# Kernel tuning notes

Hardware: AMD Instinct MI355X
Metric: run time of the kernel (lower is better)

Reference implementation:

```python
import jax, jax.numpy as jnp
import numpy as np

EPS = 1e-5
P = 3  # p_size
BW = 1.0  # bandwidth


def _instance_norm(x):
    # calc_mean_std: per (B,C) mean/std over spatial dims, unbiased var (torch default)
    b, c, h, w = x.shape
    flat = x.reshape(b, c, h * w)
    mean = flat.mean(-1)[:, :, None, None]
    std = jnp.sqrt(flat.var(-1, ddof=1) + EPS)[:, :, None, None]
    return (x - mean) / std


def _conv1x1(x, w, bias):
    # x: (B,C,H,W), w: (O,C), bias: (O,)
    return jnp.einsum('oc,bchw->bohw', w, x) + bias[None, :, None, None]


def _patches_scaled(x, scale):
    # ReflectionPad2d(1) + Unfold(3) -> (B, HW, C*9), torch layout (c slow, k fast),
    # with ContextAtten scale applied over the 9 kernel positions.
    b, c, h, w = x.shape
    pad = jnp.pad(x, ((0, 0), (0, 0), (1, 1), (1, 1)), mode='reflect')
    # (B,C,H,W,9)
    p9 = jnp.stack([pad[:, :, di:di + h, dj:dj + w]
                    for di in range(P) for dj in range(P)], axis=-1)
    p9 = p9 * scale  # broadcast over last (kernel) axis
    # -> (B,H,W,C,9) -> (B, HW, C*9)
    return p9.transpose(0, 2, 3, 1, 4).reshape(b, h * w, c * P * P)


def setup_inputs() -> dict:
    key = jax.random.key(0)
    ks = jax.random.split(key, 12)
    B, C, H, W = 2, 512, 64, 64
    IC = 256
    f32 = jnp.float32
    inp = {
        'content': jax.random.normal(ks[0], (B, C, H, W), f32),
        'style': jax.random.normal(ks[1], (B, C, H, W), f32),
        'fusion_style': jax.random.normal(ks[2], (B, C, H, W), f32),
        'theta_w': jax.random.normal(ks[3], (IC, C), f32) * np.sqrt(2.0 / C),
        'theta_b': jnp.zeros((IC,), f32),
        'phi_w': jax.random.normal(ks[4], (IC, C), f32) * np.sqrt(2.0 / C),
        'phi_b': jnp.zeros((IC,), f32),
        'g_w': jax.random.normal(ks[5], (IC, C), f32) * np.sqrt(2.0 / C),
        'g_b': jnp.zeros((IC,), f32),
        'W_w': jax.random.normal(ks[6], (C, IC), f32) * np.sqrt(2.0 / IC),
        'W_b': jnp.zeros((C,), f32),
        'scale': jnp.ones((P * P,), f32),
    }
    return inp


def reference(content, style, fusion_style, theta_w, theta_b, phi_w, phi_b,
              g_w, g_b, W_w, W_b, scale):
    B, C, H, W = content.shape
    IC = theta_w.shape[0]
    HW = H * W

    # g on fusion_style -> (B, HW, IC)
    g_s = _conv1x1(fusion_style, g_w, g_b).reshape(B, IC, HW).transpose(0, 2, 1)

    # instance-normalize content/style (normal=True path)
    xn = _instance_norm(content)
    sn = _instance_norm(style)

    theta_x = _conv1x1(xn, theta_w, theta_b)
    phi_s = _conv1x1(sn, phi_w, phi_b)

    theta_p = _patches_scaled(theta_x, scale)  # (B, HW, IC*9)
    phi_p = _patches_scaled(phi_s, scale)      # (B, HW, IC*9)

    f = jnp.einsum('blk,bmk->blm', theta_p, phi_p) * BW  # (B, HW, HW)
    f_div_C = jax.nn.softmax(f, axis=-1)

    y = jnp.einsum('blm,bmo->blo', f_div_C, g_s)  # (B, HW, IC)
    y = y.transpose(0, 2, 1).reshape(B, IC, H, W)
    W_y = _conv1x1(y, W_w, W_b)  # (B, C, H, W)
    # isTraining=True path: conf_map = 0
    return W_y
```

## Files before the change

kernel.cpp:

```cpp
#include <hip/hip_runtime.h>
#include <stdint.h>

typedef __attribute__((ext_vector_type(8))) __bf16 bf16x8;
typedef __attribute__((ext_vector_type(4))) float f32x4;
typedef __attribute__((ext_vector_type(4))) unsigned int uint4v;
typedef __attribute__((ext_vector_type(4))) unsigned short ushort4v;
typedef __attribute__((ext_vector_type(8))) unsigned short ushort8v;

__device__ __forceinline__ float bf2f(unsigned short u){
  unsigned int x = ((unsigned int)u) << 16;
  return __builtin_bit_cast(float, x);
}
__device__ __forceinline__ unsigned short f2bf(float f){
  unsigned int x = __builtin_bit_cast(unsigned int, f);
  x += 0x7FFFu + ((x >> 16) & 1u);
  return (unsigned short)(x >> 16);
}

#define OUT_PART 4
#define OUT_PARTH 5

typedef const __attribute__((address_space(1))) unsigned int* gas1_t;
typedef __attribute__((address_space(3))) unsigned int* las3_t;
__device__ __forceinline__ void gload16(const void* g, void* l){
  __builtin_amdgcn_global_load_lds((gas1_t)g, (las3_t)l, 16, 0, 0);
}

template<int OM>
__global__ __launch_bounds__(256)
void gemm_bt(const unsigned short* __restrict__ A, int lda,
             const unsigned short* __restrict__ Bt, int ldb,
             int kchunk, void* __restrict__ Out, int ldo,
             size_t zStride, size_t aBatch, size_t bBatch,
             int sMask, int sShift)
{
  __shared__ uint4v AsmBuf[1024];
  __shared__ uint4v BsmBuf[1024];
  char* Asm = (char*)AsmBuf;
  char* Bsm = (char*)BsmBuf;

  const int tid  = threadIdx.x;
  const int lane = tid & 63;
  const int wave = tid >> 6;
  const int wy = wave >> 1, wx = wave & 1;
  const int lm = lane & 15, quad = lane >> 4;
  const int tileM = blockIdx.y * 128;
  const int tileN = blockIdx.x * 128;
  const int z = blockIdx.z;
  const int slice = z & sMask;
  const int batch = z >> sShift;

  A  += (size_t)slice*kchunk + (size_t)batch*aBatch;
  Bt += (size_t)slice*kchunk + (size_t)batch*bBatch;

  const int sr0 = tid >> 2, sc0 = tid & 3;
  const int sr1 = sr0 + 64;
  const size_t gA0 = (size_t)(tileM + sr0)*lda + ((sc0 ^ ((sr0 >> 1) & 3)) << 3);
  const size_t gA1 = (size_t)(tileM + sr1)*lda + ((sc0 ^ ((sr1 >> 1) & 3)) << 3);
  const size_t gB0 = (size_t)(tileN + sr0)*ldb + ((sc0 ^ ((sr0 >> 1) & 3)) << 3);
  const size_t gB1 = (size_t)(tileN + sr1)*ldb + ((sc0 ^ ((sr1 >> 1) & 3)) << 3);
  const int lOff0 = sr0*64 + sc0*16;
  const int lOff1 = sr1*64 + sc0*16;

  int aOff[4], bOff[4];
#pragma unroll
  for (int t = 0; t < 4; ++t){
    int ra = wy*64 + t*16 + lm;
    aOff[t] = ra*64 + ((quad ^ ((ra >> 1) & 3)) << 4);
    int rb = wx*64 + t*16 + lm;
    bOff[t] = rb*64 + ((quad ^ ((rb >> 1) & 3)) << 4);
  }

  f32x4 acc[4][4] = {};

  const int ksteps = kchunk >> 5;
  uint4v a0v = *(const uint4v*)(A + gA0);
  uint4v a1v = *(const uint4v*)(A + gA1);
  uint4v b0v = *(const uint4v*)(Bt + gB0);
  uint4v b1v = *(const uint4v*)(Bt + gB1);

  for (int kt = 0; kt < ksteps; ++kt){
    char* As = Asm + (kt & 1)*8192;
    char* Bs = Bsm + (kt & 1)*8192;
    *(uint4v*)(As + lOff0) = a0v;
    *(uint4v*)(As + lOff1) = a1v;
    *(uint4v*)(Bs + lOff0) = b0v;
    *(uint4v*)(Bs + lOff1) = b1v;
    __syncthreads();
    if (kt + 1 < ksteps){
      const unsigned short* Ak = A + (kt + 1)*32;
      const unsigned short* Bk = Bt + (kt + 1)*32;
      a0v = *(const uint4v*)(Ak + gA0);
      a1v = *(const uint4v*)(Ak + gA1);
      b0v = *(const uint4v*)(Bk + gB0);
      b1v = *(const uint4v*)(Bk + gB1);
    }
    bf16x8 af[4], bfr[4];
#pragma unroll
    for (int t = 0; t < 4; ++t){
      af[t]  = __builtin_bit_cast(bf16x8, *(const uint4v*)(As + aOff[t]));
      bfr[t] = __builtin_bit_cast(bf16x8, *(const uint4v*)(Bs + bOff[t]));
    }
#pragma unroll
    for (int tm = 0; tm < 4; ++tm)
#pragma unroll
      for (int tn = 0; tn < 4; ++tn)
        acc[tm][tn] = __builtin_amdgcn_mfma_f32_16x16x32_bf16(af[tm], bfr[tn], acc[tm][tn], 0, 0, 0);
  }

#pragma unroll
  for (int tm = 0; tm < 4; ++tm){
    const int rowb = tileM + wy*64 + tm*16 + quad*4;
#pragma unroll
    for (int tn = 0; tn < 4; ++tn){
      const int col = tileN + wx*64 + tn*16 + lm;
#pragma unroll
      for (int r = 0; r < 4; ++r){
        const float v = acc[tm][tn][r];
        const size_t idx = (size_t)z*zStride + (size_t)(rowb + r)*ldo + col;
        if (OM == OUT_PART) ((float*)Out)[idx] = v;
        else                ((unsigned short*)Out)[idx] = f2bf(v);
      }
    }
  }
}

template<int OM>
__global__ __launch_bounds__(256)
void gemm_wide(const unsigned short* __restrict__ A, int lda,
               const unsigned short* __restrict__ Bt, int ldb,
               int kchunk, void* __restrict__ Out, int ldo,
               size_t zStride, size_t aBatch, size_t bBatch,
               int sMask, int sShift)
{
  __shared__ char lds[49152];

  const int tid  = threadIdx.x;
  const int lane = tid & 63;
  const int wave = tid >> 6;
  const int wy = wave >> 1, wx = wave & 1;
  const int lm = lane & 15, quad = lane >> 4;
  const int tileM = blockIdx.y * 128;
  const int tileN = blockIdx.x * 256;
  const int z = blockIdx.z;
  const int slice = z & sMask;
  const int batch = z >> sShift;

  A  += (size_t)slice*kchunk + (size_t)batch*aBatch;
  Bt += (size_t)slice*kchunk + (size_t)batch*bBatch;

  const int srow  = tid >> 2;
  const int selem = (((tid & 3) ^ ((tid >> 3) & 3)) << 3);
  const int dst   = tid << 4;
  size_t gA[2], gB[4];
#pragma unroll
  for (int i = 0; i < 2; ++i)
    gA[i] = (size_t)(tileM + srow + 64*i)*lda + selem;
#pragma unroll
  for (int i = 0; i < 4; ++i)
    gB[i] = (size_t)(tileN + srow + 64*i)*ldb + selem;

  int aOff[4], bOff[8];
#pragma unroll
  for (int t = 0; t < 4; ++t){
    const int ra = wy*64 + t*16 + lm;
    aOff[t] = ra*64 + ((quad ^ ((ra >> 1) & 3)) << 4);
  }
#pragma unroll
  for (int t = 0; t < 8; ++t){
    const int rb = wx*128 + t*16 + lm;
    bOff[t] = rb*64 + ((quad ^ ((rb >> 1) & 3)) << 4);
  }

  f32x4 acc[4][8] = {};
  const int nk = kchunk >> 5;

#pragma unroll
  for (int i = 0; i < 2; ++i) gload16(A  + gA[i], lds + i*4096 + dst);
#pragma unroll
  for (int i = 0; i < 4; ++i) gload16(Bt + gB[i], lds + 8192 + i*4096 + dst);

  for (int kt = 0; kt < nk; ++kt){
    const char* As = lds + (kt & 1)*24576;
    const char* Bs = As + 8192;
    if (kt + 1 < nk){
      char* nbuf = lds + ((kt + 1) & 1)*24576;
      const unsigned short* Ak = A  + (size_t)(kt + 1)*32;
      const unsigned short* Bk = Bt + (size_t)(kt + 1)*32;
#pragma unroll
      for (int i = 0; i < 2; ++i) gload16(Ak + gA[i], nbuf + i*4096 + dst);
#pragma unroll
      for (int i = 0; i < 4; ++i) gload16(Bk + gB[i], nbuf + 8192 + i*4096 + dst);
      asm volatile("s_waitcnt vmcnt(6)" ::: "memory");
    } else {
      asm volatile("s_waitcnt vmcnt(0)" ::: "memory");
    }
    __builtin_amdgcn_s_barrier();
    asm volatile("" ::: "memory");

    bf16x8 af[4], bfr[8];
#pragma unroll
    for (int t = 0; t < 8; ++t)
      bfr[t] = __builtin_bit_cast(bf16x8, *(const uint4v*)(Bs + bOff[t]));
#pragma unroll
    for (int t = 0; t < 4; ++t)
      af[t] = __builtin_bit_cast(bf16x8, *(const uint4v*)(As + aOff[t]));
#pragma unroll
    for (int tm = 0; tm < 4; ++tm)
#pragma unroll
      for (int tn = 0; tn < 8; ++tn)
        acc[tm][tn] = __builtin_amdgcn_mfma_f32_16x16x32_bf16(af[tm], bfr[tn], acc[tm][tn], 0, 0, 0);

    asm volatile("" ::: "memory");
    __builtin_amdgcn_s_barrier();
  }

#pragma unroll
  for (int tm = 0; tm < 4; ++tm){
    const int rowb = tileM + wy*64 + tm*16 + quad*4;
#pragma unroll
    for (int tn = 0; tn < 8; ++tn){
      const int col = tileN + wx*128 + tn*16 + lm;
#pragma unroll
      for (int r = 0; r < 4; ++r){
        const float v = acc[tm][tn][r];
        const size_t idx = (size_t)z*zStride + (size_t)(rowb + r)*ldo + col;
        if (OM == OUT_PART) ((float*)Out)[idx] = v;
        else                ((unsigned short*)Out)[idx] = f2bf(v);
      }
    }
  }
}

__global__ __launch_bounds__(512, 2)
void gemm_big256(const unsigned short* __restrict__ A, int lda,
                 const unsigned short* __restrict__ Bt, int ldb,
                 int K, float* __restrict__ Out, int ldo,
                 size_t aBatch, size_t bBatch, size_t oBatch)
{
  __shared__ char lds[131072];

  const int tid  = threadIdx.x;
  const int lane = tid & 63;
  const int wv   = tid >> 6;
  const int wy = wv >> 2, wx = wv & 3;
  const int lm = lane & 15, quad = lane >> 4;

  const int lid = (int)(blockIdx.x + (blockIdx.y << 4) + (blockIdx.z << 8));
  const int swz = ((lid & 7) << 6) + (lid >> 3);
  const int tileM = ((swz >> 4) & 15) * 256;
  const int tileN = (swz & 15) * 256;
  const int z = swz >> 8;

  A   += (size_t)z*aBatch;
  Bt  += (size_t)z*bBatch;
  Out += (size_t)z*oBatch;

  const int srow  = tid >> 3;
  const int selem = (((tid & 7) ^ ((tid >> 3) & 7)) << 3);
  const int dst   = tid << 4;
  size_t gA[4], gB[4];
#pragma unroll
  for (int i = 0; i < 4; ++i){
    gA[i] = (size_t)(tileM + srow + 64*i)*lda + selem;
    gB[i] = (size_t)(tileN + srow + 64*i)*ldb + selem;
  }

  int xq[2];
#pragma unroll
  for (int kk = 0; kk < 2; ++kk)
    xq[kk] = ((((kk << 2) + quad) ^ (lm & 7)) << 4);
  const int aBase = (wy*128 + lm) << 7;
  const int bBase = (wx*64  + lm) << 7;

  f32x4 acc[8][4] = {};
  const int nk = K >> 6;

#pragma unroll
  for (int i = 0; i < 4; ++i) gload16(A  + gA[i], lds + i*8192 + dst);
#pragma unroll
  for (int i = 0; i < 4; ++i) gload16(Bt + gB[i], lds + 32768 + i*8192 + dst);

  for (int kt = 0; kt < nk; ++kt){
    const char* As = lds + (kt & 1)*65536;
    const char* Bs = As + 32768;
    if (kt + 1 < nk){
      char* nbuf = lds + ((kt + 1) & 1)*65536;
      const unsigned short* Ak = A  + (size_t)(kt + 1)*64;
      const unsigned short* Bk = Bt + (size_t)(kt + 1)*64;
#pragma unroll
      for (int i = 0; i < 4; ++i) gload16(Ak + gA[i], nbuf + i*8192 + dst);
#pragma unroll
      for (int i = 0; i < 4; ++i) gload16(Bk + gB[i], nbuf + 32768 + i*8192 + dst);
      asm volatile("s_waitcnt vmcnt(8)" ::: "memory");
    } else {
      asm volatile("s_waitcnt vmcnt(0)" ::: "memory");
    }
    __builtin_amdgcn_s_barrier();
    asm volatile("" ::: "memory");

#pragma unroll
    for (int kk = 0; kk < 2; ++kk){
      bf16x8 af[8], bfr[4];
#pragma unroll
      for (int n = 0; n < 4; ++n)
        bfr[n] = __builtin_bit_cast(bf16x8, *(const uint4v*)(Bs + bBase + n*2048 + xq[kk]));
#pragma unroll
      for (int m = 0; m < 8; ++m)
        af[m] = __builtin_bit_cast(bf16x8, *(const uint4v*)(As + aBase + m*2048 + xq[kk]));
#pragma unroll
      for (int m = 0; m < 8; ++m)
#pragma unroll
        for (int n = 0; n < 4; ++n)
          acc[m][n] = __builtin_amdgcn_mfma_f32_16x16x32_bf16(af[m], bfr[n], acc[m][n], 0, 0, 0);
    }

    asm volatile("" ::: "memory");
    __builtin_amdgcn_s_barrier();
  }

#pragma unroll
  for (int tm = 0; tm < 8; ++tm){
    const int rowb = tileM + wy*128 + tm*16 + quad*4;
#pragma unroll
    for (int tn = 0; tn < 4; ++tn){
      const int col = tileN + wx*64 + tn*16 + lm;
#pragma unroll
      for (int r = 0; r < 4; ++r)
        Out[(size_t)(rowb + r)*ldo + col] = acc[tm][tn][r];
    }
  }
}

__global__ __launch_bounds__(256)
void reduce_tp(const float* __restrict__ part,
               const float* __restrict__ tb, const float* __restrict__ pb,
               unsigned short* __restrict__ th, unsigned short* __restrict__ ph)
{
  const size_t i4 = ((size_t)blockIdx.x*256 + threadIdx.x) * 4;
  const int which = (int)(i4 >> 21);
  const size_t j = i4 & 0x1FFFFFu;
  const int col = (int)(j & 255u);
  f32x4 v = {0.f, 0.f, 0.f, 0.f};
#pragma unroll
  for (int s = 0; s < 4; ++s){
    f32x4 p = *(const f32x4*)&part[(size_t)((which << 2) + s)*2097152 + j];
#pragma unroll
    for (int e = 0; e < 4; ++e) v[e] += p[e];
  }
  f32x4 bv = *(const f32x4*)&(which ? pb : tb)[col];
  ushort4v hi, lo;
#pragma unroll
  for (int e = 0; e < 4; ++e){
    const float t = v[e] + bv[e];
    hi[e] = f2bf(t);
    lo[e] = f2bf(t - bf2f(hi[e]));
  }
  const size_t o = (j >> 8)*768 + col;
  unsigned short* O = which ? ph : th;
  const int dup = which ? 512 : 256;
  const int loo = which ? 256 : 512;
  *(ushort4v*)&O[o] = hi;
  *(ushort4v*)&O[o + dup] = hi;
  *(ushort4v*)&O[o + loo] = lo;
}

__global__ __launch_bounds__(256)
void reduce_g(const unsigned short* __restrict__ part,
              const float* __restrict__ gb, unsigned short* __restrict__ gs)
{
  const size_t i8 = ((size_t)blockIdx.x*256 + threadIdx.x) * 8;
  float v[8] = {};
#pragma unroll
  for (int s = 0; s < 4; ++s){
    uint4v u = *(const uint4v*)&part[(size_t)s*2097152 + i8];
#pragma unroll
    for (int e = 0; e < 8; ++e)
      v[e] += bf2f((unsigned short)((e & 1) ? (u[e >> 1] >> 16) : (u[e >> 1] & 0xffffu)));
  }
  const float gbv = gb[i8 >> 13];
  ushort8v o;
#pragma unroll
  for (int e = 0; e < 8; ++e) o[e] = f2bf(v[e] + gbv);
  *(ushort8v*)&gs[i8] = o;
}

__global__ __launch_bounds__(256)
void reduce_y(const unsigned short* __restrict__ part,
              unsigned short* __restrict__ yb)
{
  const size_t i8 = ((size_t)blockIdx.x*256 + threadIdx.x) * 8;
  const int b = (int)(i8 >> 20);
  const size_t j = i8 & 0xFFFFFu;
  float v[8] = {};
#pragma unroll
  for (int s = 0; s < 8; ++s){
    uint4v u = *(const uint4v*)&part[(size_t)((b << 3) + s)*1048576 + j];
#pragma unroll
    for (int e = 0; e < 8; ++e)
      v[e] += bf2f((unsigned short)((e & 1) ? (u[e >> 1] >> 16) : (u[e >> 1] & 0xffffu)));
  }
  ushort8v o;
#pragma unroll
  for (int e = 0; e < 8; ++e) o[e] = f2bf(v[e]);
  *(ushort8v*)&yb[i8] = o;
}

__global__ __launch_bounds__(256)
void reduce_w(const float* __restrict__ part, const float* __restrict__ wb,
              void* __restrict__ Out, const unsigned int* __restrict__ flagPtr)
{
  const size_t i4 = ((size_t)blockIdx.x*256 + threadIdx.x) * 4;
  const int b = (int)(i4 >> 21);
  const size_t j = i4 & 0x1FFFFFu;
  f32x4 p0 = *(const f32x4*)&part[(size_t)(b << 1)*2097152 + j];
  f32x4 p1 = *(const f32x4*)&part[(size_t)((b << 1) | 1)*2097152 + j];
  const float w = wb[(i4 >> 12) & 511u];
  f32x4 v;
#pragma unroll
  for (int e = 0; e < 4; ++e) v[e] = p0[e] + p1[e] + w;
  if (flagPtr[0]){
    *(f32x4*)&((float*)Out)[i4] = v;
  } else {
    ushort4v o;
#pragma unroll
    for (int e = 0; e < 4; ++e) o[e] = f2bf(v[e]);
    *(ushort4v*)&((unsigned short*)Out)[i4] = o;
  }
}

__global__ __launch_bounds__(256)
void detect_prep(const void* __restrict__ content,
                 const void* tb, const void* pb, const void* gb, const void* wb,
                 const void* sc,
                 unsigned int* __restrict__ flag, float* __restrict__ scale_c,
                 float* tb_c, float* pb_c, float* gb_c, float* wb_c)
{
  __shared__ int cnt;
  __shared__ unsigned int flg;
  const int tid = threadIdx.x;
  if (tid == 0) cnt = 0;
  __syncthreads();
  unsigned int w = ((const unsigned int*)content)[tid];
  int e = (w >> 23) & 0xFF;
  if (e >= 0x70 && e <= 0x8F) atomicAdd(&cnt, 1);
  __syncthreads();
  if (tid == 0){ flg = (cnt >= 128) ? 1u : 0u; flag[0] = flg; }
  __syncthreads();
  const unsigned int f = flg;
  auto rd = [&](const void* p, int i)->float{
    return f ? ((const float*)p)[i] : bf2f(((const unsigned short*)p)[i]);
  };
  if (tid < 9) scale_c[tid] = rd(sc, tid);
  tb_c[tid] = rd(tb, tid);
  pb_c[tid] = rd(pb, tid);
  gb_c[tid] = rd(gb, tid);
  wb_c[tid] = rd(wb, tid);
  wb_c[tid + 256] = rd(wb, tid + 256);
}

__global__ __launch_bounds__(256)
void conv_weights(const void* tw, const void* pw, const void* gw, const void* www,
                  const unsigned int* __restrict__ flagPtr,
                  unsigned short* __restrict__ wdup,
                  unsigned short* __restrict__ gwc,
                  unsigned short* __restrict__ wwc)
{
  const unsigned int fl = flagPtr[0];
  const int sec = blockIdx.y;
  const int idx = blockIdx.x*256 + threadIdx.x;
  auto rd = [&](const void* p, int i)->float{
    return fl ? ((const float*)p)[i] : bf2f(((const unsigned short*)p)[i]);
  };
  if (sec < 2){
    const void* w = sec ? pw : tw;
    const int o = idx >> 9, c = idx & 511;
    float v = rd(w, o*512 + c);
    unsigned short hi = f2bf(v);
    unsigned short lo = f2bf(v - bf2f(hi));
    unsigned short* base = wdup + (size_t)sec*256*1536 + o*1536;
    base[c] = hi; base[512 + c] = lo; base[1024 + c] = hi;
  } else if (sec == 2){
    const int o = idx >> 9, c = idx & 511;
    gwc[o*512 + c] = f2bf(rd(gw, o*512 + c));
  } else {
    const int o = idx >> 8, c = idx & 255;
    wwc[o*256 + c] = f2bf(rd(www, o*256 + c));
  }
}

__global__ __launch_bounds__(256)
void stats_all(const void* __restrict__ content, const void* __restrict__ style,
               const unsigned int* __restrict__ flagPtr,
               float* __restrict__ statsC, float* __restrict__ statsS)
{
  const unsigned int fl = flagPtr[0];
  const void* X = blockIdx.z ? style : content;
  float* stats = blockIdx.z ? statsS : statsC;
  const int bc = blockIdx.x;
  const int tid = threadIdx.x;
  float s = 0.f, q = 0.f;
  if (fl){
    const f32x4* row = (const f32x4*)((const float*)X + (size_t)bc*4096);
#pragma unroll
    for (int i = 0; i < 4; ++i){
      f32x4 v = row[tid + i*256];
#pragma unroll
      for (int j = 0; j < 4; ++j){ s += v[j]; q += v[j]*v[j]; }
    }
  } else {
    const uint4v* row = (const uint4v*)((const unsigned short*)X + (size_t)bc*4096);
#pragma unroll
    for (int i = 0; i < 2; ++i){
      uint4v u = row[tid + i*256];
#pragma unroll
      for (int j = 0; j < 4; ++j){
        float a = bf2f((unsigned short)(u[j] & 0xffffu));
        float b = bf2f((unsigned short)(u[j] >> 16));
        s += a + b; q += a*a + b*b;
      }
    }
  }
#pragma unroll
  for (int off = 32; off > 0; off >>= 1){
    s += __shfl_down(s, off);
    q += __shfl_down(q, off);
  }
  __shared__ float rs[4], rq[4];
  if ((tid & 63) == 0){ rs[tid >> 6] = s; rq[tid >> 6] = q; }
  __syncthreads();
  if (tid == 0){
    s = rs[0] + rs[1] + rs[2] + rs[3];
    q = rq[0] + rq[1] + rq[2] + rq[3];
    float mean = s * (1.0f/4096.0f);
    float var  = (q - 4096.0f*mean*mean) * (1.0f/4095.0f);
    stats[bc*2 + 0] = mean;
    stats[bc*2 + 1] = 1.0f / sqrtf(var + 1e-5f);
  }
}

__global__ __launch_bounds__(256)
void norm_all(const void* __restrict__ content, const void* __restrict__ style,
              const void* __restrict__ fusion,
              const float* __restrict__ statsC, const float* __restrict__ statsS,
              unsigned short* __restrict__ xn, unsigned short* __restrict__ sn,
              unsigned short* __restrict__ fst,
              const unsigned int* __restrict__ flagPtr)
{
  __shared__ float tile[64][65];
  const unsigned int fl = flagPtr[0];
  const int z = blockIdx.z;
  const int which = z >> 1;
  const int b  = z & 1;
  const int l0 = blockIdx.x * 64;
  const int c0 = blockIdx.y * 64;
  const int tid = threadIdx.x;
  const int tx = tid & 63, ty = tid >> 6;

  const void* X = which == 0 ? content : (which == 1 ? style : fusion);
#pragma unroll
  for (int p = 0; p < 16; ++p){
    const int cc = ty + p*4;
    const size_t src = ((size_t)b*512 + c0 + cc)*4096 + l0 + tx;
    tile[cc][tx] = fl ? ((const float*)X)[src]
                      : bf2f(((const unsigned short*)X)[src]);
  }
  __syncthreads();
  if (which < 2){
    const float* stats = which ? statsS : statsC;
    const float mean = stats[(b*512 + c0 + tx)*2 + 0];
    const float inv  = stats[(b*512 + c0 + tx)*2 + 1];
    unsigned short* Out = which ? sn : xn;
#pragma unroll
    for (int p = 0; p < 16; ++p){
      const int lj = ty + p*4;
      const float v = (tile[tx][lj] - mean) * inv;
      const size_t o = ((size_t)b*4096 + l0 + lj)*1536 + c0 + tx;
      const unsigned short hi = f2bf(v);
      Out[o] = hi;
      Out[o + 512] = hi;
      Out[o + 1024] = f2bf(v - bf2f(hi));
    }
  } else {
#pragma unroll
    for (int p = 0; p < 16; ++p){
      const int lj = ty + p*4;
      const size_t o = ((size_t)b*4096 + l0 + lj)*512 + c0 + tx;
      fst[o] = f2bf(tile[tx][lj]);
    }
  }
}

__global__ __launch_bounds__(256)
void softmax_rows(const float* __restrict__ Gbase, const float* __restrict__ scale_c,
                  unsigned short* __restrict__ Pbase)
{
  const int bid = (int)((blockIdx.x & 7)*1024 + (blockIdx.x >> 3));
  const int bb = bid >> 12;
  const int l  = bid & 4095;
  const float* G = Gbase + (size_t)bb*16777216;
  unsigned short* P = Pbase + (size_t)bb*16777216;
  const int yy = l >> 6, xx = l & 63;
  const int tid = threadIdx.x;

  float s2[9];
  const float* rowp[9];
#pragma unroll
  for (int di = 0; di < 3; ++di){
    int ry = yy + di - 1; ry = ry < 0 ? 1 : (ry > 63 ? 62 : ry);
#pragma unroll
    for (int dj = 0; dj < 3; ++dj){
      int rx = xx + dj - 1; rx = rx < 0 ? 1 : (rx > 63 ? 62 : rx);
      const int k = di*3 + dj;
      const float s = scale_c[k];
      s2[k] = s*s;
      rowp[k] = G + (size_t)(ry*64 + rx)*4096;
    }
  }

  const int mxo = tid & 63, my0 = tid >> 6;
  int cx[3];
#pragma unroll
  for (int d = 0; d < 3; ++d){
    int t1 = mxo + d - 1;
    cx[d] = (t1 < 0 ? 1 : (t1 > 63 ? 62 : t1));
  }

  float fv[16];
  float mx = -3.0e38f;
#pragma unroll
  for (int i = 0; i < 16; ++i){
    const int my = my0 + i*4;
    int cy[3];
#pragma unroll
    for (int d = 0; d < 3; ++d){
      int t0 = my + d - 1;
      cy[d] = (t0 < 0 ? 1 : (t0 > 63 ? 62 : t0))*64;
    }
    float v = 0.f;
#pragma unroll
    for (int di = 0; di < 3; ++di)
#pragma unroll
      for (int dj = 0; dj < 3; ++dj)
        v = fmaf(s2[di*3+dj], rowp[di*3+dj][cy[di] + cx[dj]], v);
    fv[i] = v;
    mx = fmaxf(mx, v);
  }

  __shared__ float redA[4], redB[4];
#pragma unroll
  for (int off = 32; off > 0; off >>= 1) mx = fmaxf(mx, __shfl_down(mx, off));
  if ((tid & 63) == 0) redA[tid >> 6] = mx;
  __syncthreads();
  mx = fmaxf(fmaxf(redA[0], redA[1]), fmaxf(redA[2], redA[3]));

  float sum = 0.f;
#pragma unroll
  for (int i = 0; i < 16; ++i){ fv[i] = __expf(fv[i] - mx); sum += fv[i]; }
#pragma unroll
  for (int off = 32; off > 0; off >>= 1) sum += __shfl_down(sum, off);
  if ((tid & 63) == 0) redB[tid >> 6] = sum;
  __syncthreads();
  sum = redB[0] + redB[1] + redB[2] + redB[3];
  const float inv = 1.0f / sum;

  unsigned short* Prow = P + (size_t)l*4096;
#pragma unroll
  for (int i = 0; i < 16; ++i) Prow[tid + i*256] = f2bf(fv[i]*inv);
}

extern "C" void kernel_launch(void* const* d_in, const int* in_sizes, int n_in,
                              void* d_out, int out_size, void* d_ws, size_t ws_size,
                              hipStream_t stream)
{
  const void* content = d_in[0];
  const void* style   = d_in[1];
  const void* fusion  = d_in[2];
  const void* theta_w = d_in[3];
  const void* theta_b = d_in[4];
  const void* phi_w   = d_in[5];
  const void* phi_b   = d_in[6];
  const void* g_w     = d_in[7];
  const void* g_b     = d_in[8];
  const void* W_w     = d_in[9];
  const void* W_b     = d_in[10];
  const void* scale   = d_in[11];

  char* ws = (char*)d_ws;
  size_t off = 0;
  auto take = [&](size_t bytes)->char*{
    char* p = ws + off; off += (bytes + 255) & ~(size_t)255; return p;
  };

  unsigned int* flag  = (unsigned int*)take(256);
  float* scale_c      = (float*)take(256);
  float* tb_c         = (float*)take(1024);
  float* pb_c         = (float*)take(1024);
  float* gb_c         = (float*)take(1024);
  float* wb_c         = (float*)take(2048);
  float* statsC       = (float*)take(1024ull*2*4);
  float* statsS       = (float*)take(1024ull*2*4);
  unsigned short* wdup = (unsigned short*)take(2ull*256*1536*2);
  unsigned short* gwc  = (unsigned short*)take(256ull*512*2);
  unsigned short* wwc  = (unsigned short*)take(512ull*256*2);
  unsigned short* th   = (unsigned short*)take(8192ull*768*2);
  unsigned short* ph   = (unsigned short*)take(8192ull*768*2);
  unsigned short* gs   = (unsigned short*)take(256ull*8192*2);
  unsigned short* yb   = (unsigned short*)take(2ull*4096*256*2);
  float* G0            = (float*)take(4096ull*4096*4);
  float* G1            = (float*)take(4096ull*4096*4);
  char* unionC         = take(64ull*1024*1024);
  unsigned short* xn   = (unsigned short*)unionC;
  unsigned short* sn   = (unsigned short*)(unionC + 8192ull*1536*2);
  unsigned short* fst  = (unsigned short*)(unionC + 2ull*8192*1536*2);
  unsigned short* P    = (unsigned short*)unionC;

  float* partTP          = G0;
  unsigned short* partG  = (unsigned short*)G1;
  unsigned short* partY  = (unsigned short*)G0;
  float* partW           = G1;

  detect_prep<<<1, 256, 0, stream>>>(content, theta_b, phi_b, g_b, W_b, scale,
                                     flag, scale_c, tb_c, pb_c, gb_c, wb_c);
  conv_weights<<<dim3(512,4), 256, 0, stream>>>(theta_w, phi_w, g_w, W_w, flag,
                                                wdup, gwc, wwc);
  stats_all<<<dim3(1024,1,2), 256, 0, stream>>>(content, style, flag, statsC, statsS);
  norm_all<<<dim3(64,8,6), 256, 0, stream>>>(content, style, fusion,
                                             statsC, statsS, xn, sn, fst, flag);

  gemm_wide<OUT_PART><<<dim3(1,64,8), 256, 0, stream>>>(
      xn, 1536, wdup, 1536, 384, partTP, 256, 8192ull*256,
      8192ull*1536, 256ull*1536, 3, 2);
  reduce_tp<<<4096, 256, 0, stream>>>(partTP, tb_c, pb_c, th, ph);

  gemm_bt<OUT_PARTH><<<dim3(64,2,4), 256, 0, stream>>>(
      gwc, 512, fst, 512, 128, partG, 8192, 256ull*8192, 0, 0, 3, 2);
  reduce_g<<<1024, 256, 0, stream>>>(partG, gb_c, gs);

  gemm_big256<<<dim3(16,16,2), 512, 0, stream>>>(
      th, 768, ph, 768, 768, G0, 4096,
      4096ull*768, 4096ull*768, (size_t)(G1 - G0));

  softmax_rows<<<8192, 256, 0, stream>>>(G0, scale_c, P);

  gemm_wide<OUT_PARTH><<<dim3(1,32,16), 256, 0, stream>>>(
      P, 4096, gs, 8192, 512, partY, 256, 4096ull*256,
      16777216ull, 4096ull, 7, 3);
  reduce_y<<<1024, 256, 0, stream>>>(partY, yb);

  gemm_bt<OUT_PART><<<dim3(32,4,4), 256, 0, stream>>>(
      wwc, 256, yb, 256, 128, partW, 4096, 512ull*4096,
      0, 4096ull*256, 1, 1);
  reduce_w<<<4096, 256, 0, stream>>>(partW, wb_c, d_out, flag);
}
```

Measured before the change: 359.3 us.

## Split GEMM mainloop into four quadrant phases interleaving loads with MFMA

Result: no change. 360.4 us (+0.3%).

```diff
diff --git a/kernel.cpp b/kernel.cpp
--- a/kernel.cpp
+++ b/kernel.cpp
@@ -245,77 +245,153 @@
   const int wv   = tid >> 6;
   const int wy = wv >> 2, wx = wv & 3;
   const int lm = lane & 15, quad = lane >> 4;
-
-  const int lid = (int)(blockIdx.x + (blockIdx.y << 4) + (blockIdx.z << 8));
-  const int swz = ((lid & 7) << 6) + (lid >> 3);
-  const int tileM = ((swz >> 4) & 15) * 256;
-  const int tileN = (swz & 15) * 256;
-  const int z = swz >> 8;
+  const int tileM = blockIdx.y * 256;
+  const int tileN = blockIdx.x * 256;
+  const int z = blockIdx.z;
 
   A   += (size_t)z*aBatch;
   Bt  += (size_t)z*bBatch;
   Out += (size_t)z*oBatch;
 
-  const int srow  = tid >> 3;
-  const int selem = (((tid & 7) ^ ((tid >> 3) & 7)) << 3);
-  const int dst   = tid << 4;
-  size_t gA[4], gB[4];
-#pragma unroll
-  for (int i = 0; i < 4; ++i){
-    gA[i] = (size_t)(tileM + srow + 64*i)*lda + selem;
-    gB[i] = (size_t)(tileN + srow + 64*i)*ldb + selem;
-  }
-
-  int xq[2];
+  const int rp0 = tid >> 3;
+  const int cg  = (((tid & 7) ^ ((tid >> 3) & 7)) << 3);
+  const int dst = tid << 4;
+  const size_t eA0[2] = { (size_t)(tileM + rp0)*lda + cg,
+                          (size_t)(tileM + 128 + rp0)*lda + cg };
+  const size_t eA1[2] = { (size_t)(tileM + 64 + rp0)*lda + cg,
+                          (size_t)(tileM + 192 + rp0)*lda + cg };
+  const int rb0 = ((rp0 >> 5) << 6) + (rp0 & 31);
+  const int rb1 = (((rp0 + 64) >> 5) << 6) + ((rp0 + 64) & 31);
+  const size_t eB0[2] = { (size_t)(tileN + rb0)*ldb + cg,
+                          (size_t)(tileN + rb1)*ldb + cg };
+  const size_t eB1[2] = { (size_t)(tileN + rb0 + 32)*ldb + cg,
+                          (size_t)(tileN + rb1 + 32)*ldb + cg };
+
+  int aR[8], bR[4], csw[2];
+#pragma unroll
+  for (int m = 0; m < 8; ++m)
+    aR[m] = (((wy << 6) + ((m & 3) << 4) + ((m >> 2) << 7) + lm) << 7);
+#pragma unroll
+  for (int n = 0; n < 4; ++n)
+    bR[n] = (((wx << 5) + ((n & 1) << 4) + ((n >> 1) << 7) + lm) << 7);
 #pragma unroll
   for (int kk = 0; kk < 2; ++kk)
-    xq[kk] = ((((kk << 2) + quad) ^ (lm & 7)) << 4);
-  const int aBase = (wy*128 + lm) << 7;
-  const int bBase = (wx*64  + lm) << 7;
+    csw[kk] = ((((kk << 2) + quad) ^ (lm & 7)) << 4);
 
   f32x4 acc[8][4] = {};
-  const int nk = K >> 6;
-
-#pragma unroll
-  for (int i = 0; i < 4; ++i) gload16(A  + gA[i], lds + i*8192 + dst);
-#pragma unroll
-  for (int i = 0; i < 4; ++i) gload16(Bt + gB[i], lds + 32768 + i*8192 + dst);
-
-  for (int kt = 0; kt < nk; ++kt){
-    const char* As = lds + (kt & 1)*65536;
+  const int nt = K >> 6;
+
+  gload16(A  + eA0[0], lds + dst);
+  gload16(A  + eA0[1], lds + 8192 + dst);
+  gload16(Bt + eB0[0], lds + 32768 + dst);
+  gload16(Bt + eB0[1], lds + 32768 + 8192 + dst);
+  gload16(Bt + eB1[0], lds + 32768 + 16384 + dst);
+  gload16(Bt + eB1[1], lds + 32768 + 16384 + 8192 + dst);
+  gload16(A  + eA1[0], lds + 16384 + dst);
+  gload16(A  + eA1[1], lds + 16384 + 8192 + dst);
+  asm volatile("s_waitcnt vmcnt(4)" ::: "memory");
+  __builtin_amdgcn_s_barrier();
+
+  for (int t = 0; t < nt; ++t){
+    const char* As = lds + (t & 1)*65536;
     const char* Bs = As + 32768;
-    if (kt + 1 < nk){
-      char* nbuf = lds + ((kt + 1) & 1)*65536;
-      const unsigned short* Ak = A  + (size_t)(kt + 1)*64;
-      const unsigned short* Bk = Bt + (size_t)(kt + 1)*64;
-#pragma unroll
-      for (int i = 0; i < 4; ++i) gload16(Ak + gA[i], nbuf + i*8192 + dst);
-#pragma unroll
-      for (int i = 0; i < 4; ++i) gload16(Bk + gB[i], nbuf + 32768 + i*8192 + dst);
-      asm volatile("s_waitcnt vmcnt(8)" ::: "memory");
-    } else {
-      asm volatile("s_waitcnt vmcnt(0)" ::: "memory");
-    }
-    __builtin_amdgcn_s_barrier();
-    asm volatile("" ::: "memory");
-
-#pragma unroll
-    for (int kk = 0; kk < 2; ++kk){
-      bf16x8 af[8], bfr[4];
-#pragma unroll
-      for (int n = 0; n < 4; ++n)
-        bfr[n] = __builtin_bit_cast(bf16x8, *(const uint4v*)(Bs + bBase + n*2048 + xq[kk]));
-#pragma unroll
-      for (int m = 0; m < 8; ++m)
-        af[m] = __builtin_bit_cast(bf16x8, *(const uint4v*)(As + aBase + m*2048 + xq[kk]));
-#pragma unroll
-      for (int m = 0; m < 8; ++m)
-#pragma unroll
-        for (int n = 0; n < 4; ++n)
-          acc[m][n] = __builtin_amdgcn_mfma_f32_16x16x32_bf16(af[m], bfr[n], acc[m][n], 0, 0, 0);
-    }
-
-    asm volatile("" ::: "memory");
+    char* nxt = lds + ((t + 1) & 1)*65536;
+    const bool hn = (t + 1 < nt);
+    const unsigned short* An = A  + (size_t)(t + 1)*64;
+    const unsigned short* Bn = Bt + (size_t)(t + 1)*64;
+
+    bf16x8 aw[4][2], bw[4][2];
+
+#pragma unroll
+    for (int m = 0; m < 4; ++m)
+#pragma unroll
+      for (int kk = 0; kk < 2; ++kk)
+        aw[m][kk] = __builtin_bit_cast(bf16x8, *(const uint4v*)(As + aR[m] + csw[kk]));
+#pragma unroll
+    for (int n = 0; n < 2; ++n)
+#pragma unroll
+      for (int kk = 0; kk < 2; ++kk)
+        bw[n][kk] = __builtin_bit_cast(bf16x8, *(const uint4v*)(Bs + bR[n] + csw[kk]));
+    if (hn){
+      gload16(An + eA0[0], nxt + dst);
+      gload16(An + eA0[1], nxt + 8192 + dst);
+    }
+    __builtin_amdgcn_s_barrier();
+    asm volatile("s_waitcnt lgkmcnt(0)" ::: "memory");
+    __builtin_amdgcn_s_setprio(1);
+#pragma unroll
+    for (int m = 0; m < 4; ++m)
+#pragma unroll
+      for (int n = 0; n < 2; ++n)
+#pragma unroll
+        for (int kk = 0; kk < 2; ++kk)
+          acc[m][n] = __builtin_amdgcn_mfma_f32_16x16x32_bf16(aw[m][kk], bw[n][kk], acc[m][n], 0, 0, 0);
+    __builtin_amdgcn_s_setprio(0);
+    if (hn) asm volatile("s_waitcnt vmcnt(4)" ::: "memory");
+    else    asm volatile("s_waitcnt vmcnt(2)" ::: "memory");
+    __builtin_amdgcn_s_barrier();
+
+#pragma unroll
+    for (int n = 2; n < 4; ++n)
+#pragma unroll
+      for (int kk = 0; kk < 2; ++kk)
+        bw[n][kk] = __builtin_bit_cast(bf16x8, *(const uint4v*)(Bs + bR[n] + csw[kk]));
+    if (hn){
+      gload16(Bn + eB0[0], nxt + 32768 + dst);
+      gload16(Bn + eB0[1], nxt + 32768 + 8192 + dst);
+    }
+    __builtin_amdgcn_s_barrier();
+    asm volatile("s_waitcnt lgkmcnt(0)" ::: "memory");
+    __builtin_amdgcn_s_setprio(1);
+#pragma unroll
+    for (int m = 0; m < 4; ++m)
+#pragma unroll
+      for (int n = 2; n < 4; ++n)
+#pragma unroll
+        for (int kk = 0; kk < 2; ++kk)
+          acc[m][n] = __builtin_amdgcn_mfma_f32_16x16x32_bf16(aw[m][kk], bw[n][kk], acc[m][n], 0, 0, 0);
+    __builtin_amdgcn_s_setprio(0);
+    if (hn) asm volatile("s_waitcnt vmcnt(4)" ::: "memory");
+    else    asm volatile("s_waitcnt vmcnt(0)" ::: "memory");
+    __builtin_amdgcn_s_barrier();
+
+#pragma unroll
+    for (int m = 0; m < 4; ++m)
+#pragma unroll
+      for (int kk = 0; kk < 2; ++kk)
+        aw[m][kk] = __builtin_bit_cast(bf16x8, *(const uint4v*)(As + aR[m + 4] + csw[kk]));
+    if (hn){
+      gload16(Bn + eB1[0], nxt + 32768 + 16384 + dst);
+      gload16(Bn + eB1[1], nxt + 32768 + 16384 + 8192 + dst);
+    }
+    __builtin_amdgcn_s_barrier();
+    asm volatile("s_waitcnt lgkmcnt(0)" ::: "memory");
+    __builtin_amdgcn_s_setprio(1);
+#pragma unroll
+    for (int m = 0; m < 4; ++m)
+#pragma unroll
+      for (int n = 2; n < 4; ++n)
+#pragma unroll
+        for (int kk = 0; kk < 2; ++kk)
+          acc[m + 4][n] = __builtin_amdgcn_mfma_f32_16x16x32_bf16(aw[m][kk], bw[n][kk], acc[m + 4][n], 0, 0, 0);
+    __builtin_amdgcn_s_setprio(0);
+    __builtin_amdgcn_s_barrier();
+
+    if (hn){
+      gload16(An + eA1[0], nxt + 16384 + dst);
+      gload16(An + eA1[1], nxt + 16384 + 8192 + dst);
+    }
+    __builtin_amdgcn_s_barrier();
+    __builtin_amdgcn_s_setprio(1);
+#pragma unroll
+    for (int m = 0; m < 4; ++m)
+#pragma unroll
+      for (int n = 0; n < 2; ++n)
+#pragma unroll
+        for (int kk = 0; kk < 2; ++kk)
+          acc[m + 4][n] = __builtin_amdgcn_mfma_f32_16x16x32_bf16(aw[m][kk], bw[n][kk], acc[m + 4][n], 0, 0, 0);
+    __builtin_amdgcn_s_setprio(0);
+    if (hn) asm volatile("s_waitcnt vmcnt(4)" ::: "memory");
     __builtin_amdgcn_s_barrier();
   }
 
```
